# Kernel tuning notes

Hardware: AMD Instinct MI355X
Metric: run time of the kernel (lower is better)

Reference implementation:

```python
import jax, jax.numpy as jnp
import numpy as np

EPS = 1e-6
K_NN = 20
ATTEN_C = 16
NEG_SLOPE = 0.2


def _normalize(v, axis, eps=1e-12):
    n = jnp.linalg.norm(v, axis=axis, keepdims=True)
    return v / jnp.maximum(n, eps)


def channel_equi_vec_normalize(x):
    # x: [B, C, 3, ...]
    x_dir = _normalize(x, axis=2)
    x_norm = jnp.linalg.norm(x, axis=2, keepdims=True)
    return x_dir * _normalize(x_norm, axis=1)


def vn_linear_leaky_relu(x, Wf, Wd, slope=NEG_SLOPE):
    # x: [B, Cin, 3, ...]; Wf, Wd: [Cout, Cin]
    p = jnp.einsum('oi,bi...->bo...', Wf, x)
    d = jnp.einsum('oi,bi...->bo...', Wd, x)
    dot = (p * d).sum(2, keepdims=True)
    d2 = (d * d).sum(2, keepdims=True)
    neg = p - (dot / (d2 + EPS)) * d
    return slope * p + (1.0 - slope) * jnp.where(dot >= 0, p, neg)


def get_graph_feature(y, k):
    # y: [B, 1, 3, N] -> edge features [B, 2, 3, N, K]
    pts = y[:, 0]                                   # [B,3,N]
    xx = (pts ** 2).sum(1)                          # [B,N]
    inner = jnp.einsum('bdn,bdm->bnm', pts, pts)    # [B,N,N]
    neg_dist = 2.0 * inner - xx[:, :, None] - xx[:, None, :]
    _, idx = jax.lax.top_k(neg_dist, k)             # [B,N,K]
    feat = jnp.transpose(y, (0, 3, 1, 2))           # [B,N,C=1,3]
    nbr = jax.vmap(lambda f, i: f[i])(feat, idx)    # [B,N,K,C,3]
    center = jnp.broadcast_to(feat[:, :, None], nbr.shape)
    edge = jnp.concatenate([nbr - center, center], axis=3)  # [B,N,K,2C,3]
    return jnp.transpose(edge, (0, 3, 4, 1, 2))     # [B,2C,3,N,K]


def setup_inputs() -> dict:
    key = jax.random.key(0)
    ks = jax.random.split(key, 6)
    B, N, C = 8, 2048, 64
    return {
        'x': jax.random.normal(ks[0], (B, 3, N), dtype=jnp.float32),
        'y': jax.random.normal(ks[1], (B, 3, N), dtype=jnp.float32),
        'Wf1': jax.random.normal(ks[2], (C, 1), dtype=jnp.float32) * 0.5,
        'Wd1': jax.random.normal(ks[3], (C, 1), dtype=jnp.float32) * 0.5,
        'Wf2': jax.random.normal(ks[4], (C, 2), dtype=jnp.float32) * 0.5,
        'Wd2': jax.random.normal(ks[5], (C, 2), dtype=jnp.float32) * 0.5,
    }


def reference(x, y, Wf1, Wd1, Wf2, Wd2):
    # q branch: [B,1,3,N] -> [B,C,3,N]
    q_x = channel_equi_vec_normalize(vn_linear_leaky_relu(x[:, None], Wf1, Wd1))
    # k/v branch: kNN edge features -> VN-MLP -> [B,C,3,N,K]
    ye = get_graph_feature(y[:, None], K_NN)
    yf = vn_linear_leaky_relu(ye, Wf2, Wd2)
    # per-channel dot between normalized edge features and query
    qk = (channel_equi_vec_normalize(yf) * q_x[..., None]).sum(2)  # [B,C,N,K]
    B, C, N, K = qk.shape
    n_head = C // ATTEN_C
    qk_c = qk.reshape(B, n_head, ATTEN_C, N, K)
    atten = jax.nn.softmax(qk_c.sum(2, keepdims=True) / np.sqrt(3.0 * ATTEN_C), axis=-1)
    atten = jnp.broadcast_to(atten, qk_c.shape).reshape(B, C, N, K)[:, :, None]  # [B,C,1,N,K]
    return (atten * yf).sum(-1)  # [B,C,3,N]
```

## Files before the change

kernel.cpp:

```cpp
#include <hip/hip_runtime.h>
#include <hip/hip_bf16.h>
#include <math.h>

#define BDIM 8
#define NPTS 2048
#define KNN 20
#define NCH 64
#define EPSV 1e-6f

#define SWZ(v, code) __uint_as_float(__builtin_amdgcn_ds_swizzle(__float_as_uint(v), (code)))

__global__ __launch_bounds__(256) void fused_kernel(
    const float* __restrict__ x, const float* __restrict__ y,
    const float* __restrict__ Wf1, const float* __restrict__ Wd1,
    const float* __restrict__ Wf2, const float* __restrict__ Wd2,
    float* __restrict__ out) {
    __shared__ uint2 cand[4][64];
    __shared__ float4 gram[4][KNN][2];

    const int wave = threadIdx.x >> 6;
    const int lane = threadIdx.x & 63;
    const int n = blockIdx.x * 4 + wave;
    const int b = blockIdx.y;
    const float* yb = y + (size_t)b * 3 * NPTS;

    const float yn0 = yb[n], yn1 = yb[NPTS + n], yn2 = yb[2 * NPTS + n];
    const float xxn = yn0 * yn0 + yn1 * yn1 + yn2 * yn2;

    const int base_m = lane * 32;
    const float4* r0 = (const float4*)(yb + base_m);
    const float4* r1 = (const float4*)(yb + NPTS + base_m);
    const float4* r2 = (const float4*)(yb + 2 * NPTS + base_m);

    float dist[32];
#pragma unroll
    for (int q = 0; q < 8; ++q) {
        const float4 a0 = r0[q], a1 = r1[q], a2 = r2[q];
#define DCOMP(t, c0, c1, c2)                                              \
        dist[q * 4 + t] = 2.0f * (yn0 * (c0) + yn1 * (c1) + yn2 * (c2)) - \
                          xxn - ((c0) * (c0) + (c1) * (c1) + (c2) * (c2));
        DCOMP(0, a0.x, a1.x, a2.x)
        DCOMP(1, a0.y, a1.y, a2.y)
        DCOMP(2, a0.z, a1.z, a2.z)
        DCOMP(3, a0.w, a1.w, a2.w)
#undef DCOMP
    }

    float t0 = dist[0], t1 = -INFINITY;
#pragma unroll
    for (int j = 1; j < 32; ++j) {
        const float v = dist[j];
        const float hi = fmaxf(t0, v), lo = fminf(t0, v);
        t0 = hi;
        t1 = fmaxf(t1, lo);
    }

    float key = t1;
#pragma unroll
    for (int size = 2; size <= 64; size <<= 1) {
#pragma unroll
        for (int stride = size >> 1; stride > 0; stride >>= 1) {
            const float other = __shfl_xor(key, stride);
            const bool low = (lane & stride) == 0;
            const bool up = (lane & size) == 0;
            key = (low == up) ? fmaxf(key, other) : fminf(key, other);
        }
    }
    const float tau = __shfl(key, 9);

    unsigned cmask = 0u;
    int lc = 0;
#pragma unroll
    for (int j = 0; j < 32; ++j)
        if (dist[j] >= tau) { cmask |= (1u << j); ++lc; }

    int incl = lc;
#pragma unroll
    for (int off = 1; off < 64; off <<= 1) {
        const int t = __shfl_up(incl, off);
        if (lane >= off) incl += t;
    }
    const int cbase = incl - lc;
    const int C = __shfl(incl, 63);

    if (C <= 64) {
        int slot = cbase;
#pragma unroll
        for (int j = 0; j < 32; ++j) {
            if (cmask & (1u << j)) {
                cand[wave][slot] = make_uint2(__float_as_uint(dist[j]),
                                              (unsigned)(base_m + j));
                ++slot;
            }
        }
    }
    __syncthreads();

    int mk = 0;
    if (C <= 64) {
        const int t = (lane < C) ? lane : 0;
        const uint2 e = cand[wave][t];
        unsigned uv = e.x;
        uv = (uv & 0x80000000u) ? ~uv : (uv | 0x80000000u);
        unsigned long long kk = ((unsigned long long)(~uv) << 32) | (unsigned long long)e.y;
        if (lane >= C) kk = ~0ULL;
#pragma unroll
        for (int size = 2; size <= 64; size <<= 1) {
#pragma unroll
            for (int stride = size >> 1; stride > 0; stride >>= 1) {
                const unsigned long long o = __shfl_xor(kk, stride);
                const bool low = (lane & stride) == 0;
                const bool up = (lane & size) == 0;
                kk = (low == up) ? (kk < o ? kk : o) : (kk > o ? kk : o);
            }
        }
        mk = (int)(kk & 0xffffffffu);
    } else {
        int my_sel = 0;
        for (int i = 0; i < KNN; ++i) {
            float bv = dist[0];
            int bj = 0;
#pragma unroll
            for (int j = 1; j < 32; ++j)
                if (dist[j] > bv) { bv = dist[j]; bj = j; }
            int bm = base_m + bj;
            for (int off = 32; off > 0; off >>= 1) {
                const float ov = __shfl_xor(bv, off);
                const int om = __shfl_xor(bm, off);
                if (ov > bv || (ov == bv && om < bm)) { bv = ov; bm = om; }
            }
            if ((bm >> 5) == lane) {
                const int jw = bm & 31;
#pragma unroll
                for (int jj = 0; jj < 32; ++jj)
                    if (jj == jw) dist[jj] = -INFINITY;
            }
            if (lane == i) my_sel = bm;
        }
        mk = my_sel;
    }

    const int c = lane;
    const float x0 = x[((size_t)b * 3 + 0) * NPTS + n];
    const float x1 = x[((size_t)b * 3 + 1) * NPTS + n];
    const float x2 = x[((size_t)b * 3 + 2) * NPTS + n];
    const float xx = x0 * x0 + x1 * x1 + x2 * x2;
    const float yy = xxn;
    const float yx = yn0 * x0 + yn1 * x1 + yn2 * x2;

    const float f = Wf1[c], g = Wd1[c];
    const float dot1 = f * g * xx;
    const float d21 = g * g * xx;
    const float coef1 = dot1 / (d21 + EPSV);
    const float s_neg = f - coef1 * g;
    const float sxc = 0.2f * f + 0.8f * ((dot1 >= 0.0f) ? f : s_neg);
    const float qn2 = sxc * sxc * xx;
    float totq = qn2;
    totq += SWZ(totq, 0x041F);
    totq += SWZ(totq, 0x081F);
    totq += SWZ(totq, 0x101F);
    totq += SWZ(totq, 0x201F);
    totq += SWZ(totq, 0x401F);
    totq += __shfl_xor(totq, 32);
    const float qn = sqrtf(qn2);
    const float qscale = (1.0f / fmaxf(qn, 1e-12f)) * (qn / fmaxf(sqrtf(totq), 1e-12f));
    const float qs = sxc * qscale;

    if (lane < KNN) {
        const float e0 = yb[mk] - yn0;
        const float e1 = yb[NPTS + mk] - yn1;
        const float e2 = yb[2 * NPTS + mk] - yn2;
        gram[wave][lane][0] = make_float4(e0 * e0 + e1 * e1 + e2 * e2,
                                          e0 * yn0 + e1 * yn1 + e2 * yn2,
                                          e0 * x0 + e1 * x1 + e2 * x2, 0.0f);
        gram[wave][lane][1] = make_float4(e0, e1, e2, 0.0f);
    }
    __syncthreads();

    const float wf0 = Wf2[2 * c], wf1v = Wf2[2 * c + 1];
    const float wd0 = Wd2[2 * c], wd1v = Wd2[2 * c + 1];
    const float cA = wf0 * wd0, cB = wf0 * wd1v + wf1v * wd0, cC = wf1v * wd1v;
    const float dA = wd0 * wd0, dB = 2.0f * wd0 * wd1v, dC = wd1v * wd1v;

    float u[KNN], t2[KNN], hh[KNN];
#pragma unroll
    for (int k = 0; k < KNN; ++k) {
        const float4 gv = gram[wave][k][0];
        const float ee = gv.x, ey = gv.y, ex = gv.z;
        const float dt = cA * ee + cB * ey + cC * yy;
        const float dd = dA * ee + dB * ey + dC * yy;
        const float cf = dt * __builtin_amdgcn_rcpf(dd + EPSV);
        const float uu = (dt < 0.0f) ? 0.8f * cf : 0.0f;
        u[k] = uu;
        const float a = wf0 - uu * wd0;
        const float bb = wf1v - uu * wd1v;
        t2[k] = a * (a * ee + bb * ey) + bb * (a * ey + bb * yy);
        hh[k] = qs * (a * ex + bb * yx);
    }

#pragma unroll
    for (int k = 0; k < KNN; ++k) t2[k] += SWZ(t2[k], 0x041F);
#pragma unroll
    for (int k = 0; k < KNN; ++k) t2[k] += SWZ(t2[k], 0x081F);
#pragma unroll
    for (int k = 0; k < KNN; ++k) t2[k] += SWZ(t2[k], 0x101F);
#pragma unroll
    for (int k = 0; k < KNN; ++k) t2[k] += SWZ(t2[k], 0x201F);
#pragma unroll
    for (int k = 0; k < KNN; ++k) t2[k] += SWZ(t2[k], 0x401F);
#pragma unroll
    for (int k = 0; k < KNN; ++k) t2[k] += __shfl_xor(t2[k], 32);
#pragma unroll
    for (int k = 0; k < KNN; ++k) hh[k] += SWZ(hh[k], 0x041F);
#pragma unroll
    for (int k = 0; k < KNN; ++k) hh[k] += SWZ(hh[k], 0x081F);
#pragma unroll
    for (int k = 0; k < KNN; ++k) hh[k] += SWZ(hh[k], 0x101F);
#pragma unroll
    for (int k = 0; k < KNN; ++k) hh[k] += SWZ(hh[k], 0x201F);

    float att[KNN];
    float mx = -INFINITY;
#pragma unroll
    for (int k = 0; k < KNN; ++k) {
        const float rs = __builtin_amdgcn_rsqf(fmaxf(t2[k], 1e-24f));
        att[k] = hh[k] * rs * 0.14433756729740643f;
        mx = fmaxf(mx, att[k]);
    }
    float se = 0.0f;
#pragma unroll
    for (int k = 0; k < KNN; ++k) {
        att[k] = __expf(att[k] - mx);
        se += att[k];
    }
    const float inv = __builtin_amdgcn_rcpf(se);

    float o0 = 0.0f, o1 = 0.0f, o2 = 0.0f, bs = 0.0f;
#pragma unroll
    for (int k = 0; k < KNN; ++k) {
        const float4 ev = gram[wave][k][1];
        const float a = wf0 - u[k] * wd0;
        const float bb = wf1v - u[k] * wd1v;
        const float w = att[k] * inv;
        const float wa = w * a;
        bs += w * bb;
        o0 += wa * ev.x;
        o1 += wa * ev.y;
        o2 += wa * ev.z;
    }

    float* ob = out + (((size_t)b * NCH + c) * 3) * NPTS + n;
    ob[0] = o0 + bs * yn0;
    ob[NPTS] = o1 + bs * yn1;
    ob[2 * NPTS] = o2 + bs * yn2;
}

extern "C" void kernel_launch(void* const* d_in, const int* in_sizes, int n_in,
                              void* d_out, int out_size, void* d_ws, size_t ws_size,
                              hipStream_t stream) {
    const float* x = (const float*)d_in[0];
    const float* y = (const float*)d_in[1];
    const float* Wf1 = (const float*)d_in[2];
    const float* Wd1 = (const float*)d_in[3];
    const float* Wf2 = (const float*)d_in[4];
    const float* Wd2 = (const float*)d_in[5];
    float* out = (float*)d_out;

    dim3 grid(NPTS / 4, BDIM);
    fused_kernel<<<grid, 256, 0, stream>>>(x, y, Wf1, Wd1, Wf2, Wd2, out);
}
```

Before: 149.8 us.

## Precompute point norms, ballot-based candidate compaction, rank selection, drop block syncs

Adds a small pre-kernel that computes squared norms of all y points into workspace, so the distance loop becomes three FMAs with the top-2 tracking fused in. Candidate compaction now uses ballot and mbcnt instead of a shuffle prefix scan. The 64-wide 64-bit bitonic sort is replaced by an O(C) rank count through LDS that writes neighbour indices directly. The q-branch computation is hoisted earlier and both __syncthreads are removed, relying on per-wave LDS usage. The risks are an extra kernel launch, missing wave-level barriers around the LDS handoff, and dropping the -xxn term, which does not change the ranking.

```diff
diff --git a/kernel.cpp b/kernel.cpp
--- a/kernel.cpp
+++ b/kernel.cpp
@@ -10,49 +10,83 @@
 
 #define SWZ(v, code) __uint_as_float(__builtin_amdgcn_ds_swizzle(__float_as_uint(v), (code)))
 
+__global__ __launch_bounds__(256) void xx_kernel(const float* __restrict__ y,
+                                                 float* __restrict__ xx) {
+    const int t = blockIdx.x * 256 + threadIdx.x;
+    const int b = t >> 11, m = t & (NPTS - 1);
+    const float* yb = y + (size_t)b * 3 * NPTS;
+    const float a = yb[m], c = yb[NPTS + m], d = yb[2 * NPTS + m];
+    xx[t] = a * a + c * c + d * d;
+}
+
 __global__ __launch_bounds__(256) void fused_kernel(
     const float* __restrict__ x, const float* __restrict__ y,
     const float* __restrict__ Wf1, const float* __restrict__ Wd1,
     const float* __restrict__ Wf2, const float* __restrict__ Wd2,
-    float* __restrict__ out) {
-    __shared__ uint2 cand[4][64];
+    const float* __restrict__ xx, float* __restrict__ out) {
+    __shared__ uint2 cand[4][128];
     __shared__ float4 gram[4][KNN][2];
+    __shared__ int knn_lds[4][KNN];
 
     const int wave = threadIdx.x >> 6;
     const int lane = threadIdx.x & 63;
     const int n = blockIdx.x * 4 + wave;
     const int b = blockIdx.y;
     const float* yb = y + (size_t)b * 3 * NPTS;
+    const float* xxb = xx + (size_t)b * NPTS;
 
     const float yn0 = yb[n], yn1 = yb[NPTS + n], yn2 = yb[2 * NPTS + n];
+    const float y20 = 2.0f * yn0, y21 = 2.0f * yn1, y22 = 2.0f * yn2;
     const float xxn = yn0 * yn0 + yn1 * yn1 + yn2 * yn2;
+
+    const int c = lane;
+    const float x0 = x[((size_t)b * 3 + 0) * NPTS + n];
+    const float x1 = x[((size_t)b * 3 + 1) * NPTS + n];
+    const float x2 = x[((size_t)b * 3 + 2) * NPTS + n];
+    const float xq = x0 * x0 + x1 * x1 + x2 * x2;
+    const float f = Wf1[c], g = Wd1[c];
+    const float dot1 = f * g * xq;
+    const float d21 = g * g * xq;
+    const float coef1 = dot1 / (d21 + EPSV);
+    const float s_neg = f - coef1 * g;
+    const float sxc = 0.2f * f + 0.8f * ((dot1 >= 0.0f) ? f : s_neg);
+    const float qn2 = sxc * sxc * xq;
+    float totq = qn2;
+    totq += SWZ(totq, 0x041F);
+    totq += SWZ(totq, 0x081F);
+    totq += SWZ(totq, 0x101F);
+    totq += SWZ(totq, 0x201F);
+    totq += SWZ(totq, 0x401F);
+    totq += __shfl_xor(totq, 32);
+    const float qn = sqrtf(qn2);
+    const float qscale = (1.0f / fmaxf(qn, 1e-12f)) * (qn / fmaxf(sqrtf(totq), 1e-12f));
+    const float qs = sxc * qscale;
 
     const int base_m = lane * 32;
     const float4* r0 = (const float4*)(yb + base_m);
     const float4* r1 = (const float4*)(yb + NPTS + base_m);
     const float4* r2 = (const float4*)(yb + 2 * NPTS + base_m);
+    const float4* rx = (const float4*)(xxb + base_m);
 
     float dist[32];
+    float t0 = -INFINITY, t1 = -INFINITY;
 #pragma unroll
     for (int q = 0; q < 8; ++q) {
-        const float4 a0 = r0[q], a1 = r1[q], a2 = r2[q];
-#define DCOMP(t, c0, c1, c2)                                              \
-        dist[q * 4 + t] = 2.0f * (yn0 * (c0) + yn1 * (c1) + yn2 * (c2)) - \
-                          xxn - ((c0) * (c0) + (c1) * (c1) + (c2) * (c2));
-        DCOMP(0, a0.x, a1.x, a2.x)
-        DCOMP(1, a0.y, a1.y, a2.y)
-        DCOMP(2, a0.z, a1.z, a2.z)
-        DCOMP(3, a0.w, a1.w, a2.w)
+        const float4 a0 = r0[q], a1 = r1[q], a2 = r2[q], ax = rx[q];
+#define DCOMP(t, c0, c1, c2, xm)                                          \
+        {                                                                  \
+            const float d = fmaf(y20, (c0),                                \
+                            fmaf(y21, (c1), fmaf(y22, (c2), -(xm))));      \
+            dist[q * 4 + t] = d;                                           \
+            const float hi = fmaxf(t0, d), lo = fminf(t0, d);              \
+            t0 = hi;                                                       \
+            t1 = fmaxf(t1, lo);                                            \
+        }
+        DCOMP(0, a0.x, a1.x, a2.x, ax.x)
+        DCOMP(1, a0.y, a1.y, a2.y, ax.y)
+        DCOMP(2, a0.z, a1.z, a2.z, ax.z)
+        DCOMP(3, a0.w, a1.w, a2.w, ax.w)
 #undef DCOMP
-    }
-
-    float t0 = dist[0], t1 = -INFINITY;
-#pragma unroll
-    for (int j = 1; j < 32; ++j) {
-        const float v = dist[j];
-        const float hi = fmaxf(t0, v), lo = fminf(t0, v);
-        t0 = hi;
-        t1 = fmaxf(t1, lo);
     }
 
     float key = t1;
@@ -68,55 +102,34 @@
     }
     const float tau = __shfl(key, 9);
 
-    unsigned cmask = 0u;
-    int lc = 0;
-#pragma unroll
-    for (int j = 0; j < 32; ++j)
-        if (dist[j] >= tau) { cmask |= (1u << j); ++lc; }
-
-    int incl = lc;
-#pragma unroll
-    for (int off = 1; off < 64; off <<= 1) {
-        const int t = __shfl_up(incl, off);
-        if (lane >= off) incl += t;
-    }
-    const int cbase = incl - lc;
-    const int C = __shfl(incl, 63);
+    int wbase = 0;
+#pragma unroll
+    for (int j = 0; j < 32; ++j) {
+        const bool pred = dist[j] >= tau;
+        const unsigned long long bal = __ballot(pred);
+        const int off = (int)__builtin_amdgcn_mbcnt_hi(
+            (unsigned)(bal >> 32),
+            __builtin_amdgcn_mbcnt_lo((unsigned)bal, 0u));
+        const int slot = wbase + off;
+        const int idx = (pred && slot < 64) ? slot : (64 + lane);
+        cand[wave][idx] = make_uint2(__float_as_uint(dist[j]),
+                                     (unsigned)(base_m + j));
+        wbase += (int)__popcll(bal);
+    }
+    const int C = wbase;
 
     if (C <= 64) {
-        int slot = cbase;
-#pragma unroll
-        for (int j = 0; j < 32; ++j) {
-            if (cmask & (1u << j)) {
-                cand[wave][slot] = make_uint2(__float_as_uint(dist[j]),
-                                              (unsigned)(base_m + j));
-                ++slot;
-            }
-        }
-    }
-    __syncthreads();
-
-    int mk = 0;
-    if (C <= 64) {
-        const int t = (lane < C) ? lane : 0;
-        const uint2 e = cand[wave][t];
-        unsigned uv = e.x;
-        uv = (uv & 0x80000000u) ? ~uv : (uv | 0x80000000u);
-        unsigned long long kk = ((unsigned long long)(~uv) << 32) | (unsigned long long)e.y;
-        if (lane >= C) kk = ~0ULL;
-#pragma unroll
-        for (int size = 2; size <= 64; size <<= 1) {
-#pragma unroll
-            for (int stride = size >> 1; stride > 0; stride >>= 1) {
-                const unsigned long long o = __shfl_xor(kk, stride);
-                const bool low = (lane & stride) == 0;
-                const bool up = (lane & size) == 0;
-                kk = (low == up) ? (kk < o ? kk : o) : (kk > o ? kk : o);
-            }
-        }
-        mk = (int)(kk & 0xffffffffu);
+        const uint2 e = cand[wave][(lane < C) ? lane : 0];
+        const float v = __uint_as_float(e.x);
+        const int mm = (int)e.y;
+        int rank = 0;
+        for (int s = 0; s < C; ++s) {
+            const uint2 o = cand[wave][s];
+            const float ov = __uint_as_float(o.x);
+            rank += (ov > v || (ov == v && (int)o.y < mm)) ? 1 : 0;
+        }
+        if (lane < C && rank < KNN) knn_lds[wave][rank] = mm;
     } else {
-        int my_sel = 0;
         for (int i = 0; i < KNN; ++i) {
             float bv = dist[0];
             int bj = 0;
@@ -135,38 +148,15 @@
                 for (int jj = 0; jj < 32; ++jj)
                     if (jj == jw) dist[jj] = -INFINITY;
             }
-            if (lane == i) my_sel = bm;
-        }
-        mk = my_sel;
-    }
-
-    const int c = lane;
-    const float x0 = x[((size_t)b * 3 + 0) * NPTS + n];
-    const float x1 = x[((size_t)b * 3 + 1) * NPTS + n];
-    const float x2 = x[((size_t)b * 3 + 2) * NPTS + n];
-    const float xx = x0 * x0 + x1 * x1 + x2 * x2;
+            if (lane == 0) knn_lds[wave][i] = bm;
+        }
+    }
+
     const float yy = xxn;
     const float yx = yn0 * x0 + yn1 * x1 + yn2 * x2;
 
-    const float f = Wf1[c], g = Wd1[c];
-    const float dot1 = f * g * xx;
-    const float d21 = g * g * xx;
-    const float coef1 = dot1 / (d21 + EPSV);
-    const float s_neg = f - coef1 * g;
-    const float sxc = 0.2f * f + 0.8f * ((dot1 >= 0.0f) ? f : s_neg);
-    const float qn2 = sxc * sxc * xx;
-    float totq = qn2;
-    totq += SWZ(totq, 0x041F);
-    totq += SWZ(totq, 0x081F);
-    totq += SWZ(totq, 0x101F);
-    totq += SWZ(totq, 0x201F);
-    totq += SWZ(totq, 0x401F);
-    totq += __shfl_xor(totq, 32);
-    const float qn = sqrtf(qn2);
-    const float qscale = (1.0f / fmaxf(qn, 1e-12f)) * (qn / fmaxf(sqrtf(totq), 1e-12f));
-    const float qs = sxc * qscale;
-
     if (lane < KNN) {
+        const int mk = knn_lds[wave][lane];
         const float e0 = yb[mk] - yn0;
         const float e1 = yb[NPTS + mk] - yn1;
         const float e2 = yb[2 * NPTS + mk] - yn2;
@@ -175,7 +165,6 @@
                                           e0 * x0 + e1 * x1 + e2 * x2, 0.0f);
         gram[wave][lane][1] = make_float4(e0, e1, e2, 0.0f);
     }
-    __syncthreads();
 
     const float wf0 = Wf2[2 * c], wf1v = Wf2[2 * c + 1];
     const float wd0 = Wd2[2 * c], wd1v = Wd2[2 * c + 1];
@@ -265,7 +254,9 @@
     const float* Wf2 = (const float*)d_in[4];
     const float* Wd2 = (const float*)d_in[5];
     float* out = (float*)d_out;
-
+    float* xx = (float*)d_ws;
+
+    xx_kernel<<<dim3(BDIM * NPTS / 256), 256, 0, stream>>>(y, xx);
     dim3 grid(NPTS / 4, BDIM);
-    fused_kernel<<<grid, 256, 0, stream>>>(x, y, Wf1, Wd1, Wf2, Wd2, out);
+    fused_kernel<<<grid, 256, 0, stream>>>(x, y, Wf1, Wd1, Wf2, Wd2, xx, out);
 }
```

Result: slower. 162.5 us (+8.5%).
